# Performance work log

Hardware: AMD Instinct MI355X
Metric: run time of the kernel (lower is better)

The kernel has to match this reference:

```python
import jax, jax.numpy as jnp
import numpy as np

T, B, D, H = 4096, 4, 1024, 8
EPS = 1e-5


def _ln(z, g, b):
    m = jnp.mean(z, axis=-1, keepdims=True)
    v = jnp.mean((z - m) ** 2, axis=-1, keepdims=True)
    return (z - m) * jax.lax.rsqrt(v + EPS) * g + b


def setup_inputs() -> dict:
    key = jax.random.key(0)
    ks = jax.random.split(key, 8)
    s = 0.02
    return {
        "x": jax.random.normal(ks[0], (T, B, D), dtype=jnp.float32),
        "norm_w": jnp.ones((D,), jnp.float32),
        "norm_b": jnp.zeros((D,), jnp.float32),
        "tnorm_w": jnp.ones((D,), jnp.float32),
        "tnorm_b": jnp.zeros((D,), jnp.float32),
        "Wq": jax.random.normal(ks[1], (D, D), jnp.float32) * s,
        "bq": jnp.zeros((D,), jnp.float32),
        "Wk": jax.random.normal(ks[2], (D, D), jnp.float32) * s,
        "bk": jnp.zeros((D,), jnp.float32),
        "Wv": jax.random.normal(ks[3], (D, D), jnp.float32) * s,
        "bv": jnp.zeros((D,), jnp.float32),
    }


def reference(x, norm_w, norm_b, tnorm_w, tnorm_b, Wq, bq, Wk, bk, Wv, bv):
    # x: (T, B, D) -> (B, T, D), matching torch x.permute(1, 0, 2)
    xb = jnp.transpose(x, (1, 0, 2))
    b, t, d = xb.shape
    hd = d // H
    xn = _ln(xb, norm_w, norm_b)          # query branch norm
    xtn = _ln(xb, tnorm_w, tnorm_b)       # key/value branch norm (text_norm applied to x)
    q = (xn @ Wq.T + bq).reshape(b, t, H, hd)
    k = (xtn @ Wk.T + bk).reshape(b, t, H, hd)
    v = (xtn @ Wv.T + bv).reshape(b, t, H, hd)
    q = jax.nn.softmax(q, axis=-1)        # softmax over head-dim
    k = jax.nn.softmax(k, axis=1)         # softmax over time
    # kv state: (B, H, hd, hd)
    att = jnp.einsum('bthd,bthl->bhdl', k, v)
    y = jnp.einsum('bthd,bhdl->bthl', q, att).reshape(b, t, d)
    return y  # original forward returns y directly (proj_out/dropout unused)
```

## Files before the change

kernel.cpp:

```cpp
#include <hip/hip_runtime.h>
#include <cstdint>

#define T_LEN 4096
#define BATCH 4
#define DIM   1024
#define NH    8
#define HDIM  128
#define ROWS  16384

typedef __bf16 bf16x8 __attribute__((ext_vector_type(8)));
typedef float  f32x4  __attribute__((ext_vector_type(4)));

__device__ __forceinline__ unsigned short f2bf(float f) {
  union { float f; unsigned u; } a; a.f = f;
  unsigned u = a.u;
  u += 0x7fff + ((u >> 16) & 1);
  return (unsigned short)(u >> 16);
}
__device__ __forceinline__ float bf2f(unsigned short h) {
  union { unsigned u; float f; } a; a.u = ((unsigned)h) << 16;
  return a.f;
}

__device__ __forceinline__ void gld_lds16(const unsigned short* g, unsigned short* l) {
  __builtin_amdgcn_global_load_lds(
      (const __attribute__((address_space(1))) unsigned int*)g,
      (__attribute__((address_space(3))) unsigned int*)l, 16, 0, 0);
}

__global__ __launch_bounds__(256) void ln_kernel(
    const float* __restrict__ x, const float* __restrict__ nw, const float* __restrict__ nb,
    const float* __restrict__ tw, const float* __restrict__ tb,
    unsigned short* __restrict__ xn, unsigned short* __restrict__ xtn) {
  int row = blockIdx.x;
  int t = row >> 2, b = row & 3;
  int tid = threadIdx.x;
  const float4 v = ((const float4*)(x + (size_t)row * DIM))[tid];
  float s  = v.x + v.y + v.z + v.w;
  float s2 = v.x*v.x + v.y*v.y + v.z*v.z + v.w*v.w;
#pragma unroll
  for (int o = 32; o; o >>= 1) { s += __shfl_xor(s, o); s2 += __shfl_xor(s2, o); }
  __shared__ float red[8];
  int wv = tid >> 6;
  if ((tid & 63) == 0) { red[wv] = s; red[4 + wv] = s2; }
  __syncthreads();
  s  = red[0] + red[1] + red[2] + red[3];
  s2 = red[4] + red[5] + red[6] + red[7];
  float mean = s * (1.0f / DIM);
  float var  = s2 * (1.0f / DIM) - mean * mean;
  float rstd = rsqrtf(var + 1e-5f);
  size_t orow = ((size_t)b * T_LEN + t) * DIM;
  int c0 = tid * 4;
  float xv[4] = {v.x, v.y, v.z, v.w};
  union { unsigned short u[4]; uint2 d; } o1, o2;
#pragma unroll
  for (int j = 0; j < 4; ++j) {
    int c = c0 + j;
    float xh = (xv[j] - mean) * rstd;
    o1.u[j] = f2bf(xh * nw[c] + nb[c]);
    o2.u[j] = f2bf(xh * tw[c] + tb[c]);
  }
  *(uint2*)(xn  + orow + c0) = o1.d;
  *(uint2*)(xtn + orow + c0) = o2.d;
}

__global__ __launch_bounds__(256) void wconv(
    const float* __restrict__ Wq, const float* __restrict__ Wk, const float* __restrict__ Wv,
    unsigned short* __restrict__ out) {
  int i4 = blockIdx.x * 256 + threadIdx.x;
  int w = i4 >> 18;
  const float* src = (w == 0) ? Wq : (w == 1 ? Wk : Wv);
  float4 v = ((const float4*)src)[i4 & 262143];
  union { unsigned short u[4]; uint2 d; } o;
  o.u[0] = f2bf(v.x); o.u[1] = f2bf(v.y); o.u[2] = f2bf(v.z); o.u[3] = f2bf(v.w);
  ((uint2*)out)[i4] = o.d;
}

__global__ __launch_bounds__(256) void qkv_gemm(
    const unsigned short* __restrict__ xn, const unsigned short* __restrict__ xtn,
    const unsigned short* __restrict__ wbf,
    const float* __restrict__ bq, const float* __restrict__ bk, const float* __restrict__ bv,
    unsigned short* __restrict__ qo, unsigned short* __restrict__ ko, unsigned short* __restrict__ vo) {
  int z = blockIdx.z;
  const unsigned short* A = (z == 0) ? xn : xtn;
  const unsigned short* W = wbf + (size_t)z * DIM * DIM;
  const float* bias = (z == 0) ? bq : (z == 1 ? bk : bv);
  unsigned short* outp = (z == 0) ? qo : (z == 1 ? ko : vo);

  int m0t = blockIdx.x * 128;
  int n0 = blockIdx.y * 128;
  __shared__ __align__(16) unsigned short As[128 * 64];
  __shared__ __align__(16) unsigned short Bs[128 * 64];
  int tid = threadIdx.x;
  int wave = tid >> 6, lane = tid & 63;
  int wm = (wave >> 1) * 64, wn = (wave & 1) * 64;
  int l16 = lane & 15, kq = lane >> 4;
  int swz = l16 & 7;

  int srow = tid >> 3;
  int skk  = (((tid & 7) ^ ((tid >> 3) & 7)) * 8);
  const unsigned short* Ag = A + (size_t)(m0t + srow) * DIM + skk;
  const unsigned short* Wg = W + (size_t)(n0 + srow) * DIM + skk;
  unsigned short* Al = As + wave * 512;
  unsigned short* Bl = Bs + wave * 512;

  f32x4 acc[4][4] = {};

  for (int kt = 0; kt < DIM; kt += 64) {
#pragma unroll
    for (int p = 0; p < 4; ++p) {
      gld_lds16(Ag + (size_t)(p * 32) * DIM + kt, Al + p * 2048);
      gld_lds16(Wg + (size_t)(p * 32) * DIM + kt, Bl + p * 2048);
    }
    __syncthreads();
#pragma unroll
    for (int ks4 = 0; ks4 < 2; ++ks4) {
      int coff = (((kq + ks4 * 4) ^ swz) * 8);
      bf16x8 fa[4], fb[4];
#pragma unroll
      for (int i = 0; i < 4; ++i) {
        fa[i] = *(const bf16x8*)(As + (wm + i * 16 + l16) * 64 + coff);
        fb[i] = *(const bf16x8*)(Bs + (wn + i * 16 + l16) * 64 + coff);
      }
#pragma unroll
      for (int i = 0; i < 4; ++i)
#pragma unroll
        for (int j = 0; j < 4; ++j)
          acc[i][j] = __builtin_amdgcn_mfma_f32_16x16x32_bf16(fa[i], fb[j], acc[i][j], 0, 0, 0);
    }
    __syncthreads();
  }

  float bcol[4];
#pragma unroll
  for (int j = 0; j < 4; ++j) bcol[j] = bias[n0 + wn + j * 16 + l16];
#pragma unroll
  for (int i = 0; i < 4; ++i)
#pragma unroll
    for (int j = 0; j < 4; ++j)
#pragma unroll
      for (int r = 0; r < 4; ++r) acc[i][j][r] += bcol[j];

  if (z == 0) {
    float* redm = (float*)As;
    float* reds = redm + 256;
#pragma unroll
    for (int i = 0; i < 4; ++i) {
#pragma unroll
      for (int r = 0; r < 4; ++r) {
        float pm = acc[i][0][r];
#pragma unroll
        for (int j = 1; j < 4; ++j) pm = fmaxf(pm, acc[i][j][r]);
        pm = fmaxf(pm, __shfl_xor(pm, 1));
        pm = fmaxf(pm, __shfl_xor(pm, 2));
        pm = fmaxf(pm, __shfl_xor(pm, 4));
        pm = fmaxf(pm, __shfl_xor(pm, 8));
        float ps = 0.0f;
#pragma unroll
        for (int j = 0; j < 4; ++j) ps += __expf(acc[i][j][r] - pm);
        ps += __shfl_xor(ps, 1);
        ps += __shfl_xor(ps, 2);
        ps += __shfl_xor(ps, 4);
        ps += __shfl_xor(ps, 8);
        if (l16 == 0) {
          int lrow = wm + i * 16 + kq * 4 + r;
          redm[lrow * 2 + (wave & 1)] = pm;
          reds[lrow * 2 + (wave & 1)] = ps;
        }
      }
    }
    __syncthreads();
#pragma unroll
    for (int i = 0; i < 4; ++i) {
#pragma unroll
      for (int r = 0; r < 4; ++r) {
        int lrow = wm + i * 16 + kq * 4 + r;
        float ma = redm[lrow * 2], mb = redm[lrow * 2 + 1];
        float sa = reds[lrow * 2], sb = reds[lrow * 2 + 1];
        float M = fmaxf(ma, mb);
        float inv = 1.0f / (sa * __expf(ma - M) + sb * __expf(mb - M));
        size_t gr = (size_t)(m0t + lrow) * DIM;
#pragma unroll
        for (int j = 0; j < 4; ++j) {
          int col = n0 + wn + j * 16 + l16;
          outp[gr + col] = f2bf(__expf(acc[i][j][r] - M) * inv);
        }
      }
    }
  } else {
    int b = m0t >> 12;
    int tb = m0t & 4095;
    unsigned short* obase = outp + (size_t)b * DIM * T_LEN + tb;
    bool doExp = (z == 1);
#pragma unroll
    for (int j = 0; j < 4; ++j) {
      int col = n0 + wn + j * 16 + l16;
      unsigned short* cp = obase + (size_t)col * T_LEN;
#pragma unroll
      for (int i = 0; i < 4; ++i) {
        int t0 = wm + i * 16 + kq * 4;
#pragma unroll
        for (int r = 0; r < 4; ++r) {
          float val = acc[i][j][r];
          cp[t0 + r] = f2bf(doExp ? __expf(val) : val);
        }
      }
    }
  }
}

__global__ __launch_bounds__(256) void zsum(
    const unsigned short* __restrict__ ksmT, float* __restrict__ Zk) {
  int row = blockIdx.x;
  const unsigned short* p = ksmT + (size_t)row * T_LEN + threadIdx.x * 16;
  uint4 a = *(const uint4*)p;
  uint4 bq = *(const uint4*)(p + 8);
  const unsigned short* ua = (const unsigned short*)&a;
  const unsigned short* ub = (const unsigned short*)&bq;
  float s = 0.0f;
#pragma unroll
  for (int j = 0; j < 8; ++j) s += bf2f(ua[j]) + bf2f(ub[j]);
#pragma unroll
  for (int o = 32; o; o >>= 1) s += __shfl_xor(s, o);
  __shared__ float red[4];
  int wv = threadIdx.x >> 6;
  if ((threadIdx.x & 63) == 0) red[wv] = s;
  __syncthreads();
  if (threadIdx.x == 0) Zk[row] = red[0] + red[1] + red[2] + red[3];
}

__global__ __launch_bounds__(256) void att_gemm(
    const unsigned short* __restrict__ vT, const unsigned short* __restrict__ ksmT,
    float* __restrict__ attT) {
  int kc = blockIdx.x;
  int bh = blockIdx.y;
  const unsigned short* Arow = vT   + (size_t)bh * HDIM * T_LEN;
  const unsigned short* Brow = ksmT + (size_t)bh * HDIM * T_LEN;
  __shared__ __align__(16) unsigned short As[128 * 64];
  __shared__ __align__(16) unsigned short Bs[128 * 64];
  int tid = threadIdx.x;
  int wave = tid >> 6, lane = tid & 63;
  int wm = (wave >> 1) * 64, wn = (wave & 1) * 64;
  int l16 = lane & 15, kq = lane >> 4;
  int swz = l16 & 7;
  int srow = tid >> 3;
  int skk = (((tid & 7) ^ ((tid >> 3) & 7)) * 8);
  const unsigned short* Ag = Arow + (size_t)srow * T_LEN + skk;
  const unsigned short* Bg = Brow + (size_t)srow * T_LEN + skk;
  unsigned short* Al = As + wave * 512;
  unsigned short* Bl = Bs + wave * 512;
  f32x4 acc[4][4] = {};
  int kbeg = kc * 512;
  for (int kt = kbeg; kt < kbeg + 512; kt += 64) {
#pragma unroll
    for (int p = 0; p < 4; ++p) {
      gld_lds16(Ag + (size_t)(p * 32) * T_LEN + kt, Al + p * 2048);
      gld_lds16(Bg + (size_t)(p * 32) * T_LEN + kt, Bl + p * 2048);
    }
    __syncthreads();
#pragma unroll
    for (int ks4 = 0; ks4 < 2; ++ks4) {
      int coff = (((kq + ks4 * 4) ^ swz) * 8);
      bf16x8 fa[4], fb[4];
#pragma unroll
      for (int i = 0; i < 4; ++i) {
        fa[i] = *(const bf16x8*)(As + (wm + i * 16 + l16) * 64 + coff);
        fb[i] = *(const bf16x8*)(Bs + (wn + i * 16 + l16) * 64 + coff);
      }
#pragma unroll
      for (int i = 0; i < 4; ++i)
#pragma unroll
        for (int j = 0; j < 4; ++j)
          acc[i][j] = __builtin_amdgcn_mfma_f32_16x16x32_bf16(fa[i], fb[j], acc[i][j], 0, 0, 0);
    }
    __syncthreads();
  }
#pragma unroll
  for (int j = 0; j < 4; ++j) {
    int col = wn + j * 16 + l16;
#pragma unroll
    for (int i = 0; i < 4; ++i) {
      int rb = wm + i * 16 + kq * 4;
#pragma unroll
      for (int r = 0; r < 4; ++r)
        atomicAdd(attT + (size_t)bh * 16384 + (size_t)(rb + r) * 128 + col, acc[i][j][r]);
    }
  }
}

__global__ __launch_bounds__(256) void attcvt(
    const float* __restrict__ attT, const float* __restrict__ Zk,
    unsigned short* __restrict__ attbf) {
  int idx = blockIdx.x * 256 + threadIdx.x;
  int bh = idx >> 14;
  int b = bh >> 3, h = bh & 7;
  int d = idx & 127;
  float z = Zk[b * DIM + h * HDIM + d];
  attbf[idx] = f2bf(attT[idx] / z);
}

__global__ __launch_bounds__(256) void y_gemm(
    const unsigned short* __restrict__ qsm, const unsigned short* __restrict__ attbf,
    float* __restrict__ out) {
  int h = blockIdx.y;
  int m0t = blockIdx.x * 128;
  int b = m0t >> 12;
  int bh = b * 8 + h;
  const unsigned short* Brow = attbf + (size_t)bh * 16384;
  __shared__ __align__(16) unsigned short As[128 * 64];
  __shared__ __align__(16) unsigned short Bs[128 * 64];
  int tid = threadIdx.x;
  int wave = tid >> 6, lane = tid & 63;
  int wm = (wave >> 1) * 64, wn = (wave & 1) * 64;
  int l16 = lane & 15, kq = lane >> 4;
  int swz = l16 & 7;
  int srow = tid >> 3;
  int skk = (((tid & 7) ^ ((tid >> 3) & 7)) * 8);
  const unsigned short* Ag = qsm + (size_t)(m0t + srow) * DIM + h * HDIM + skk;
  const unsigned short* Bg = Brow + (size_t)srow * HDIM + skk;
  unsigned short* Al = As + wave * 512;
  unsigned short* Bl = Bs + wave * 512;
  f32x4 acc[4][4] = {};
  for (int kt = 0; kt < HDIM; kt += 64) {
#pragma unroll
    for (int p = 0; p < 4; ++p) {
      gld_lds16(Ag + (size_t)(p * 32) * DIM + kt, Al + p * 2048);
      gld_lds16(Bg + (size_t)(p * 32) * HDIM + kt, Bl + p * 2048);
    }
    __syncthreads();
#pragma unroll
    for (int ks4 = 0; ks4 < 2; ++ks4) {
      int coff = (((kq + ks4 * 4) ^ swz) * 8);
      bf16x8 fa[4], fb[4];
#pragma unroll
      for (int i = 0; i < 4; ++i) {
        fa[i] = *(const bf16x8*)(As + (wm + i * 16 + l16) * 64 + coff);
        fb[i] = *(const bf16x8*)(Bs + (wn + i * 16 + l16) * 64 + coff);
      }
#pragma unroll
      for (int i = 0; i < 4; ++i)
#pragma unroll
        for (int j = 0; j < 4; ++j)
          acc[i][j] = __builtin_amdgcn_mfma_f32_16x16x32_bf16(fa[i], fb[j], acc[i][j], 0, 0, 0);
    }
    __syncthreads();
  }
#pragma unroll
  for (int j = 0; j < 4; ++j) {
    int col = wn + j * 16 + l16;
#pragma unroll
    for (int i = 0; i < 4; ++i) {
      int rb = wm + i * 16 + kq * 4;
#pragma unroll
      for (int r = 0; r < 4; ++r)
        out[(size_t)(m0t + rb + r) * DIM + h * HDIM + col] = acc[i][j][r];
    }
  }
}

extern "C" void kernel_launch(void* const* d_in, const int* in_sizes, int n_in,
                              void* d_out, int out_size, void* d_ws, size_t ws_size,
                              hipStream_t stream) {
  const float* x  = (const float*)d_in[0];
  const float* nw = (const float*)d_in[1];
  const float* nb = (const float*)d_in[2];
  const float* tw = (const float*)d_in[3];
  const float* tb = (const float*)d_in[4];
  const float* Wq = (const float*)d_in[5];
  const float* bq = (const float*)d_in[6];
  const float* Wk = (const float*)d_in[7];
  const float* bk = (const float*)d_in[8];
  const float* Wv = (const float*)d_in[9];
  const float* bv = (const float*)d_in[10];
  float* out = (float*)d_out;

  char* ws = (char*)d_ws;
  unsigned short* xn   = (unsigned short*)(ws);
  unsigned short* xtn  = (unsigned short*)(ws + 33554432);
  unsigned short* q    = (unsigned short*)(ws + 67108864);
  unsigned short* ksmT = (unsigned short*)(ws + 100663296);
  unsigned short* vT   = (unsigned short*)(ws + 134217728);
  unsigned short* wbf  = (unsigned short*)(ws + 167772160);
  float* attT          = (float*)(ws + 174063616);
  unsigned short* attbf= (unsigned short*)(ws + 176160768);
  float* Zk            = (float*)(ws + 177209344);

  ln_kernel<<<ROWS, 256, 0, stream>>>(x, nw, nb, tw, tb, xn, xtn);
  wconv<<<3072, 256, 0, stream>>>(Wq, Wk, Wv, wbf);
  qkv_gemm<<<dim3(128, 8, 3), 256, 0, stream>>>(xn, xtn, wbf, bq, bk, bv, q, ksmT, vT);
  zsum<<<4096, 256, 0, stream>>>(ksmT, Zk);
  (void)hipMemsetAsync(attT, 0, 32 * 128 * 128 * 4, stream);
  att_gemm<<<dim3(8, 32), 256, 0, stream>>>(vT, ksmT, attT);
  attcvt<<<2048, 256, 0, stream>>>(attT, Zk, attbf);
  y_gemm<<<dim3(128, 8), 256, 0, stream>>>(q, attbf, out);
}
```

Before: 338.1 us.

## Template QKV GEMM per projection, stage transposed stores in LDS, fuse key-sum

The fused z-indexed QKV GEMM is split into three template-specialised launches. The K and V epilogues now transpose through shared memory so that global writes are coalesced 16-byte row stores instead of scattered 2-byte stores. The key softmax denominator is accumulated with atomics inside the K epilogue, which removes the separate zsum kernel. The att_gemm split-K is also doubled to 16 chunks for more parallelism, at the cost of more atomic accumulation traffic and a larger shared-memory footprint in the GEMM.

```diff
diff --git a/kernel.cpp b/kernel.cpp
--- a/kernel.cpp
+++ b/kernel.cpp
@@ -76,21 +76,16 @@
   ((uint2*)out)[i4] = o.d;
 }
 
+template<int MODE>
 __global__ __launch_bounds__(256) void qkv_gemm(
-    const unsigned short* __restrict__ xn, const unsigned short* __restrict__ xtn,
-    const unsigned short* __restrict__ wbf,
-    const float* __restrict__ bq, const float* __restrict__ bk, const float* __restrict__ bv,
-    unsigned short* __restrict__ qo, unsigned short* __restrict__ ko, unsigned short* __restrict__ vo) {
-  int z = blockIdx.z;
-  const unsigned short* A = (z == 0) ? xn : xtn;
-  const unsigned short* W = wbf + (size_t)z * DIM * DIM;
-  const float* bias = (z == 0) ? bq : (z == 1 ? bk : bv);
-  unsigned short* outp = (z == 0) ? qo : (z == 1 ? ko : vo);
-
+    const unsigned short* __restrict__ A, const unsigned short* __restrict__ W,
+    const float* __restrict__ bias,
+    unsigned short* __restrict__ outp, float* __restrict__ Zk) {
   int m0t = blockIdx.x * 128;
   int n0 = blockIdx.y * 128;
-  __shared__ __align__(16) unsigned short As[128 * 64];
-  __shared__ __align__(16) unsigned short Bs[128 * 64];
+  __shared__ __align__(16) unsigned short smem[128 * 136];
+  unsigned short* As = smem;
+  unsigned short* Bs = smem + 8192;
   int tid = threadIdx.x;
   int wave = tid >> 6, lane = tid & 63;
   int wm = (wave >> 1) * 64, wn = (wave & 1) * 64;
@@ -141,8 +136,8 @@
 #pragma unroll
       for (int r = 0; r < 4; ++r) acc[i][j][r] += bcol[j];
 
-  if (z == 0) {
-    float* redm = (float*)As;
+  if (MODE == 0) {
+    float* redm = (float*)smem;
     float* reds = redm + 256;
 #pragma unroll
     for (int i = 0; i < 4; ++i) {
@@ -188,45 +183,42 @@
       }
     }
   } else {
-    int b = m0t >> 12;
-    int tb = m0t & 4095;
-    unsigned short* obase = outp + (size_t)b * DIM * T_LEN + tb;
-    bool doExp = (z == 1);
+    unsigned short* Ts = smem;
 #pragma unroll
     for (int j = 0; j < 4; ++j) {
-      int col = n0 + wn + j * 16 + l16;
-      unsigned short* cp = obase + (size_t)col * T_LEN;
+      int col = wn + j * 16 + l16;
 #pragma unroll
       for (int i = 0; i < 4; ++i) {
         int t0 = wm + i * 16 + kq * 4;
-#pragma unroll
-        for (int r = 0; r < 4; ++r) {
-          float val = acc[i][j][r];
-          cp[t0 + r] = f2bf(doExp ? __expf(val) : val);
-        }
-      }
-    }
-  }
-}
-
-__global__ __launch_bounds__(256) void zsum(
-    const unsigned short* __restrict__ ksmT, float* __restrict__ Zk) {
-  int row = blockIdx.x;
-  const unsigned short* p = ksmT + (size_t)row * T_LEN + threadIdx.x * 16;
-  uint4 a = *(const uint4*)p;
-  uint4 bq = *(const uint4*)(p + 8);
-  const unsigned short* ua = (const unsigned short*)&a;
-  const unsigned short* ub = (const unsigned short*)&bq;
-  float s = 0.0f;
-#pragma unroll
-  for (int j = 0; j < 8; ++j) s += bf2f(ua[j]) + bf2f(ub[j]);
-#pragma unroll
-  for (int o = 32; o; o >>= 1) s += __shfl_xor(s, o);
-  __shared__ float red[4];
-  int wv = threadIdx.x >> 6;
-  if ((threadIdx.x & 63) == 0) red[wv] = s;
-  __syncthreads();
-  if (threadIdx.x == 0) Zk[row] = red[0] + red[1] + red[2] + red[3];
+        float v0 = acc[i][j][0], v1 = acc[i][j][1], v2 = acc[i][j][2], v3 = acc[i][j][3];
+        if (MODE == 1) { v0 = __expf(v0); v1 = __expf(v1); v2 = __expf(v2); v3 = __expf(v3); }
+        unsigned lo = (unsigned)f2bf(v0) | ((unsigned)f2bf(v1) << 16);
+        unsigned hi = (unsigned)f2bf(v2) | ((unsigned)f2bf(v3) << 16);
+        *(unsigned*)(Ts + col * 136 + t0)     = lo;
+        *(unsigned*)(Ts + col * 136 + t0 + 2) = hi;
+      }
+    }
+    __syncthreads();
+    int col_o = tid >> 1;
+    int th = (tid & 1) * 64;
+    int b = m0t >> 12, tb = m0t & 4095;
+    unsigned short* cp = outp + ((size_t)b * DIM + n0 + col_o) * T_LEN + tb + th;
+    float zs = 0.0f;
+#pragma unroll
+    for (int c = 0; c < 8; ++c) {
+      uint4 d = *(const uint4*)(Ts + col_o * 136 + th + c * 8);
+      *(uint4*)(cp + c * 8) = d;
+      if (MODE == 1) {
+        const unsigned short* u = (const unsigned short*)&d;
+#pragma unroll
+        for (int e = 0; e < 8; ++e) zs += bf2f(u[e]);
+      }
+    }
+    if (MODE == 1) {
+      zs += __shfl_xor(zs, 1);
+      if ((tid & 1) == 0) atomicAdd(&Zk[b * DIM + n0 + col_o], zs);
+    }
+  }
 }
 
 __global__ __launch_bounds__(256) void att_gemm(
@@ -250,8 +242,8 @@
   unsigned short* Al = As + wave * 512;
   unsigned short* Bl = Bs + wave * 512;
   f32x4 acc[4][4] = {};
-  int kbeg = kc * 512;
-  for (int kt = kbeg; kt < kbeg + 512; kt += 64) {
+  int kbeg = kc * 256;
+  for (int kt = kbeg; kt < kbeg + 256; kt += 64) {
 #pragma unroll
     for (int p = 0; p < 4; ++p) {
       gld_lds16(Ag + (size_t)(p * 32) * T_LEN + kt, Al + p * 2048);
@@ -382,15 +374,16 @@
   unsigned short* vT   = (unsigned short*)(ws + 134217728);
   unsigned short* wbf  = (unsigned short*)(ws + 167772160);
   float* attT          = (float*)(ws + 174063616);
-  unsigned short* attbf= (unsigned short*)(ws + 176160768);
-  float* Zk            = (float*)(ws + 177209344);
-
+  float* Zk            = (float*)(ws + 176160768);
+  unsigned short* attbf= (unsigned short*)(ws + 176177152);
+
+  (void)hipMemsetAsync(attT, 0, 32 * 128 * 128 * 4 + BATCH * DIM * 4, stream);
   ln_kernel<<<ROWS, 256, 0, stream>>>(x, nw, nb, tw, tb, xn, xtn);
   wconv<<<3072, 256, 0, stream>>>(Wq, Wk, Wv, wbf);
-  qkv_gemm<<<dim3(128, 8, 3), 256, 0, stream>>>(xn, xtn, wbf, bq, bk, bv, q, ksmT, vT);
-  zsum<<<4096, 256, 0, stream>>>(ksmT, Zk);
-  (void)hipMemsetAsync(attT, 0, 32 * 128 * 128 * 4, stream);
-  att_gemm<<<dim3(8, 32), 256, 0, stream>>>(vT, ksmT, attT);
+  qkv_gemm<1><<<dim3(128, 8), 256, 0, stream>>>(xtn, wbf + (size_t)1 * DIM * DIM, bk, ksmT, Zk);
+  qkv_gemm<2><<<dim3(128, 8), 256, 0, stream>>>(xtn, wbf + (size_t)2 * DIM * DIM, bv, vT, Zk);
+  qkv_gemm<0><<<dim3(128, 8), 256, 0, stream>>>(xn,  wbf,                         bq, q,  Zk);
+  att_gemm<<<dim3(16, 32), 256, 0, stream>>>(vT, ksmT, attT);
   attcvt<<<2048, 256, 0, stream>>>(attT, Zk, attbf);
   y_gemm<<<dim3(128, 8), 256, 0, stream>>>(q, attbf, out);
 }
```

New measurement: 358.6 us. 1.06x slower.
